# Kernel optimization log

Measured on AMD Instinct MI355X. Metric: run time of the kernel, lower is better.

The kernel has to match this reference:

```python
import jax, jax.numpy as jnp
import numpy as np

DIM = 1024
N_HEADS = 16
HEAD_DIM = DIM // N_HEADS
HIDDEN = 2816
SEQ = 4096
BATCH = 1
NORM_EPS = 1e-5


def setup_inputs() -> dict:
    key = jax.random.key(0)
    ks = jax.random.split(key, 9)
    s = 1.0 / np.sqrt(DIM)
    return {
        "x": jax.random.normal(ks[0], (BATCH, SEQ, DIM), jnp.float32),
        "wq": jax.random.normal(ks[1], (DIM, DIM), jnp.float32) * s,
        "wk": jax.random.normal(ks[2], (DIM, DIM), jnp.float32) * s,
        "wv": jax.random.normal(ks[3], (DIM, DIM), jnp.float32) * s,
        "wo": jax.random.normal(ks[4], (DIM, DIM), jnp.float32) * s,
        "w1": jax.random.normal(ks[5], (DIM, HIDDEN), jnp.float32) * s,
        "w2": jax.random.normal(ks[6], (HIDDEN, DIM), jnp.float32) / np.sqrt(HIDDEN),
        "w3": jax.random.normal(ks[7], (DIM, HIDDEN), jnp.float32) * s,
        "g_attn_norm": jnp.ones((DIM,), jnp.float32),
        "g_ffn_norm": jnp.ones((DIM,), jnp.float32),
    }


def rmsnorm(x, g):
    # x: [b, s, d]; compute in fp32 as in the torch module, then cast back
    xf = x.astype(jnp.float32)
    n = xf * jax.lax.rsqrt(jnp.mean(xf * xf, axis=-1, keepdims=True) + NORM_EPS)
    return n.astype(x.dtype) * g


def attention(x, wq, wk, wv, wo):
    b, s, _ = x.shape
    q = (x @ wq).reshape(b, s, N_HEADS, HEAD_DIM).transpose(0, 2, 1, 3)  # [b,h,s,hd]
    k = (x @ wk).reshape(b, s, N_HEADS, HEAD_DIM).transpose(0, 2, 1, 3)
    v = (x @ wv).reshape(b, s, N_HEADS, HEAD_DIM).transpose(0, 2, 1, 3)
    scores = jnp.einsum("bhqd,bhkd->bhqk", q, k) / np.sqrt(HEAD_DIM)
    causal = jnp.tril(jnp.ones((s, s), bool))
    scores = jnp.where(causal, scores, -jnp.inf)
    probs = jax.nn.softmax(scores.astype(jnp.float32), axis=-1).astype(q.dtype)
    out = jnp.einsum("bhqk,bhkd->bhqd", probs, v)
    out = out.transpose(0, 2, 1, 3).reshape(b, s, DIM)
    return out @ wo


def feed_forward(x, w1, w2, w3):
    return (jax.nn.silu(x @ w1) * (x @ w3)) @ w2


def reference(x, wq, wk, wv, wo, w1, w2, w3, g_attn_norm, g_ffn_norm):
    h = x + attention(rmsnorm(x, g_attn_norm), wq, wk, wv, wo)
    out = h + feed_forward(rmsnorm(h, g_ffn_norm), w1, w2, w3)
    return out
```

## Files before the change

### kernel.cpp

```cpp
#include <hip/hip_runtime.h>
#include <stdint.h>


typedef unsigned short u16;
typedef unsigned int u32;
typedef __attribute__((ext_vector_type(8))) short short8;
typedef __attribute__((ext_vector_type(4))) float f32x4;

#define GLD16(G, L) __builtin_amdgcn_global_load_lds( \
    (__attribute__((address_space(1))) void*)(G),      \
    (__attribute__((address_space(3))) void*)(L), 16, 0, 0)

__device__ __forceinline__ u16 f2bf(float f) {
  u32 u = __builtin_bit_cast(u32, f);
  u32 r = u + 0x7fffu + ((u >> 16) & 1u);
  return (u16)(r >> 16);
}
__device__ __forceinline__ float bf2f(u16 b) {
  u32 u = (u32)b << 16;
  return __builtin_bit_cast(float, u);
}

__global__ __launch_bounds__(256) void k_tc4(const float* __restrict__ s0,
                                             const float* __restrict__ s1,
                                             const float* __restrict__ s2,
                                             const float* __restrict__ s3,
                                             u16* __restrict__ out, int R, int C) {
  const int z = blockIdx.z;
  const float* in = (z == 0) ? s0 : (z == 1) ? s1 : (z == 2) ? s2 : s3;
  u16* o = out + (size_t)z * R * C;
  __shared__ float t[32][33];
  const int tx = threadIdx.x & 31, ty = threadIdx.x >> 5;
  const int c0 = blockIdx.x * 32, r0 = blockIdx.y * 32;
#pragma unroll
  for (int i = 0; i < 32; i += 8)
    t[ty + i][tx] = in[(size_t)(r0 + ty + i) * C + (c0 + tx)];
  __syncthreads();
#pragma unroll
  for (int i = 0; i < 32; i += 8)
    o[(size_t)(c0 + ty + i) * R + (r0 + tx)] = f2bf(t[tx][ty + i]);
}

__global__ __launch_bounds__(256) void k_rms(const float* __restrict__ x,
                                             const float* __restrict__ g,
                                             u16* __restrict__ o) {
  const int row = blockIdx.x, tid = threadIdx.x;
  const float4 v = ((const float4*)(x + (size_t)row * 1024))[tid];
  float ss = v.x * v.x + v.y * v.y + v.z * v.z + v.w * v.w;
#pragma unroll
  for (int ofs = 32; ofs > 0; ofs >>= 1) ss += __shfl_xor(ss, ofs);
  __shared__ float red[4];
  if ((tid & 63) == 0) red[tid >> 6] = ss;
  __syncthreads();
  const float s = rsqrtf((red[0] + red[1] + red[2] + red[3]) * (1.f / 1024.f) + 1e-5f);
  const float4 gv = ((const float4*)g)[tid];
  u32 lo = (u32)f2bf(v.x * s * gv.x) | ((u32)f2bf(v.y * s * gv.y) << 16);
  u32 hi = (u32)f2bf(v.z * s * gv.z) | ((u32)f2bf(v.w * s * gv.w) << 16);
  *(uint2*)(o + (size_t)row * 1024 + tid * 4) = make_uint2(lo, hi);
}

template <int EPI, int TN>
__global__ __launch_bounds__(256) void k_gemm(const u16* __restrict__ A,
                                              const u16* __restrict__ Bt,
                                              u16* __restrict__ Obf,
                                              float* __restrict__ Of,
                                              const float* __restrict__ Rz,
                                              int M, int N, int K) {
  constexpr int NFR = TN / 32;
  __shared__ __align__(16) u16 As[128 * 32];
  __shared__ __align__(16) u16 Bs[TN * 32];
  const int tid = threadIdx.x;
  const int lane = tid & 63, wave = tid >> 6;
  const int wr = wave >> 1, wc = wave & 1;
  const int li = lane & 15, lg = lane >> 4;
  const int row0 = blockIdx.y * 128, col0 = blockIdx.x * TN;

  f32x4 acc[4][NFR] = {};
  const int sr = tid >> 2, sc = (tid & 3) * 8;
  const u16* ag = A + (size_t)(row0 + sr) * K + sc;
  const u16* bg = Bt + (size_t)(col0 + sr) * K + sc;
  u16* al = As + tid * 8;
  u16* bl = Bs + tid * 8;
  const size_t rstep = (size_t)64 * K;

  for (int k0 = 0; k0 < K; k0 += 32) {
    __syncthreads();
    GLD16(ag + k0, al);
    GLD16(ag + rstep + k0, al + 2048);
    GLD16(bg + k0, bl);
    if constexpr (TN == 128) GLD16(bg + rstep + k0, bl + 2048);
    __syncthreads();
    short8 af[4], bfr[NFR];
#pragma unroll
    for (int m = 0; m < 4; ++m)
      af[m] = *(const short8*)(As + (wr * 64 + m * 16 + li) * 32 + lg * 8);
#pragma unroll
    for (int n = 0; n < NFR; ++n)
      bfr[n] = *(const short8*)(Bs + (wc * (TN / 2) + n * 16 + li) * 32 + lg * 8);
#pragma unroll
    for (int m = 0; m < 4; ++m)
#pragma unroll
      for (int n = 0; n < NFR; ++n)
        acc[m][n] = __builtin_amdgcn_mfma_f32_16x16x32_bf16(af[m], bfr[n], acc[m][n], 0, 0, 0);
  }

#pragma unroll
  for (int m = 0; m < 4; ++m) {
    const int row = row0 + wr * 64 + m * 16 + lg * 4;
#pragma unroll
    for (int n = 0; n < NFR; ++n) {
      const int col = col0 + wc * (TN / 2) + n * 16 + li;
#pragma unroll
      for (int r = 0; r < 4; ++r) {
        const size_t idx = (size_t)(row + r) * N + col;
        if (EPI == 0) Obf[idx] = f2bf(acc[m][n][r]);
        else          Of[idx] = acc[m][n][r] + Rz[idx];
      }
    }
  }
}

__global__ __launch_bounds__(256) void k_ffn13(const u16* __restrict__ A,
                                               const u16* __restrict__ B1,
                                               const u16* __restrict__ B3,
                                               u16* __restrict__ O,
                                               int M, int N, int K) {
  __shared__ __align__(16) u16 As[128 * 32];
  __shared__ __align__(16) u16 B1s[64 * 32];
  __shared__ __align__(16) u16 B3s[64 * 32];
  const int tid = threadIdx.x;
  const int lane = tid & 63, wave = tid >> 6;
  const int wr = wave >> 1, wc = wave & 1;
  const int li = lane & 15, lg = lane >> 4;
  const int row0 = blockIdx.y * 128, col0 = blockIdx.x * 64;

  f32x4 a1[4][2] = {}, a3[4][2] = {};
  const int sr = tid >> 2, sc = (tid & 3) * 8;
  const u16* ag = A + (size_t)(row0 + sr) * K + sc;
  const u16* b1g = B1 + (size_t)(col0 + sr) * K + sc;
  const u16* b3g = B3 + (size_t)(col0 + sr) * K + sc;
  u16* al = As + tid * 8;
  u16* b1l = B1s + tid * 8;
  u16* b3l = B3s + tid * 8;
  const size_t rstep = (size_t)64 * K;

  for (int k0 = 0; k0 < K; k0 += 32) {
    __syncthreads();
    GLD16(ag + k0, al);
    GLD16(ag + rstep + k0, al + 2048);
    GLD16(b1g + k0, b1l);
    GLD16(b3g + k0, b3l);
    __syncthreads();
    short8 af[4], b1f[2], b3f[2];
#pragma unroll
    for (int m = 0; m < 4; ++m)
      af[m] = *(const short8*)(As + (wr * 64 + m * 16 + li) * 32 + lg * 8);
#pragma unroll
    for (int n = 0; n < 2; ++n) {
      b1f[n] = *(const short8*)(B1s + (wc * 32 + n * 16 + li) * 32 + lg * 8);
      b3f[n] = *(const short8*)(B3s + (wc * 32 + n * 16 + li) * 32 + lg * 8);
    }
#pragma unroll
    for (int m = 0; m < 4; ++m)
#pragma unroll
      for (int n = 0; n < 2; ++n) {
        a1[m][n] = __builtin_amdgcn_mfma_f32_16x16x32_bf16(af[m], b1f[n], a1[m][n], 0, 0, 0);
        a3[m][n] = __builtin_amdgcn_mfma_f32_16x16x32_bf16(af[m], b3f[n], a3[m][n], 0, 0, 0);
      }
  }

#pragma unroll
  for (int m = 0; m < 4; ++m) {
    const int row = row0 + wr * 64 + m * 16 + lg * 4;
#pragma unroll
    for (int n = 0; n < 2; ++n) {
      const int col = col0 + wc * 32 + n * 16 + li;
#pragma unroll
      for (int r = 0; r < 4; ++r) {
        const float g1 = a1[m][n][r], g3 = a3[m][n][r];
        const float sl = g1 / (1.f + __expf(-g1));
        O[(size_t)(row + r) * N + col] = f2bf(sl * g3);
      }
    }
  }
}

__global__ __launch_bounds__(256) void k_attn(const u16* __restrict__ qkv,
                                              u16* __restrict__ o) {
  const int LD = 3072;
  const int h = blockIdx.x & 15;
  const int qb = 63 - (blockIdx.x >> 4);
  const int q0 = qb * 64;
  const int tid = threadIdx.x, lane = tid & 63, w = tid >> 6;
  const int li = lane & 15, lg = lane >> 4;
  const int swzB = (li & 7) << 4;

  __shared__ __align__(16) u16 Ks[64 * 64];
  __shared__ __align__(16) u16 Vt[64 * 64];
  __shared__ __align__(16) u16 Ps[4 * 16 * 64];

  const int qrow = q0 + w * 16 + li;
  const u16* qp = qkv + (size_t)qrow * LD + h * 64;
  short8 qf0, qf1;
#pragma unroll
  for (int j = 0; j < 8; ++j) {
    qf0[j] = (short)(__builtin_bit_cast(u32, bf2f(qp[lg * 8 + j]) * 0.125f) >> 16);
    qf1[j] = (short)(__builtin_bit_cast(u32, bf2f(qp[32 + lg * 8 + j]) * 0.125f) >> 16);
  }

  const int krow = w * 16 + (lane >> 3);
  const int kcol = ((lane & 7) ^ (lane >> 3)) * 8;
  const u16* kg = qkv + 1024 + h * 64 + kcol;
  u16* klds0 = Ks + (w * 2 + 0) * 512 + lane * 8;
  u16* klds1 = Ks + (w * 2 + 1) * 512 + lane * 8;

  const int vd0 = (tid & 31) * 2;
  const int vkq = tid >> 5;
  const u16* vg = qkv + 2048 + h * 64 + vd0;
  u32* vl0 = (u32*)(Vt + (size_t)vd0 * 64 + (((vkq * 16) ^ ((vd0 & 7) << 4)) >> 1));
  u32* vl1 = (u32*)(Vt + (size_t)(vd0 + 1) * 64 + (((vkq * 16) ^ (((vd0 + 1) & 7) << 4)) >> 1));

  u16* pw = Ps + w * 1024 + li * 64;

  float msm = -1e30f, lsm = 0.f;
  f32x4 accO[4] = {};
  u32 vld[8];

  {
    const u16* vp = vg;
#pragma unroll
    for (int i = 0; i < 8; ++i) vld[i] = *(const u32*)(vp + (size_t)(vkq * 8 + i) * LD);
  }

  for (int k0 = 0; k0 <= q0; k0 += 64) {
    __syncthreads();
    GLD16(kg + (size_t)(k0 + krow) * LD, klds0);
    GLD16(kg + (size_t)(k0 + krow + 8) * LD, klds1);
    {
      u32 lo0 = (vld[0] & 0xffffu) | (vld[1] << 16);
      u32 lo1 = (vld[2] & 0xffffu) | (vld[3] << 16);
      u32 lo2 = (vld[4] & 0xffffu) | (vld[5] << 16);
      u32 lo3 = (vld[6] & 0xffffu) | (vld[7] << 16);
      u32 hi0 = (vld[0] >> 16) | (vld[1] & 0xffff0000u);
      u32 hi1 = (vld[2] >> 16) | (vld[3] & 0xffff0000u);
      u32 hi2 = (vld[4] >> 16) | (vld[5] & 0xffff0000u);
      u32 hi3 = (vld[6] >> 16) | (vld[7] & 0xffff0000u);
      *(uint4*)vl0 = make_uint4(lo0, lo1, lo2, lo3);
      *(uint4*)vl1 = make_uint4(hi0, hi1, hi2, hi3);
    }
    __syncthreads();
    if (k0 + 64 <= q0) {
      const u16* vp = vg + (size_t)(k0 + 64) * LD;
#pragma unroll
      for (int i = 0; i < 8; ++i) vld[i] = *(const u32*)(vp + (size_t)(vkq * 8 + i) * LD);
    }

    f32x4 st[4];
#pragma unroll
    for (int f = 0; f < 4; ++f) {
      const u16* kp = Ks + (size_t)(f * 16 + li) * 64;
      const short8 ka0 = *(const short8*)(kp + (((lg * 16) ^ swzB) >> 1));
      const short8 ka1 = *(const short8*)(kp + (((64 + lg * 16) ^ swzB) >> 1));
      f32x4 z = {};
      z = __builtin_amdgcn_mfma_f32_16x16x32_bf16(ka0, qf0, z, 0, 0, 0);
      st[f] = __builtin_amdgcn_mfma_f32_16x16x32_bf16(ka1, qf1, z, 0, 0, 0);
    }

    float sv[16];
    float mloc = -1e30f;
    if (k0 < q0) {
#pragma unroll
      for (int f = 0; f < 4; ++f)
#pragma unroll
        for (int r = 0; r < 4; ++r) {
          sv[f * 4 + r] = st[f][r];
          mloc = fmaxf(mloc, sv[f * 4 + r]);
        }
    } else {
#pragma unroll
      for (int f = 0; f < 4; ++f)
#pragma unroll
        for (int r = 0; r < 4; ++r) {
          const int kg2 = k0 + f * 16 + lg * 4 + r;
          sv[f * 4 + r] = (kg2 > qrow) ? -1e30f : st[f][r];
          mloc = fmaxf(mloc, sv[f * 4 + r]);
        }
    }
    mloc = fmaxf(mloc, __shfl_xor(mloc, 16));
    mloc = fmaxf(mloc, __shfl_xor(mloc, 32));
    const float mnew = fmaxf(msm, mloc);
    const float alpha = __expf(msm - mnew);
    float psum = 0.f;
#pragma unroll
    for (int f = 0; f < 4; ++f) {
      const float p0 = __expf(sv[f * 4 + 0] - mnew);
      const float p1 = __expf(sv[f * 4 + 1] - mnew);
      const float p2 = __expf(sv[f * 4 + 2] - mnew);
      const float p3 = __expf(sv[f * 4 + 3] - mnew);
      psum += (p0 + p1) + (p2 + p3);
      const u32 lo = (u32)f2bf(p0) | ((u32)f2bf(p1) << 16);
      const u32 hi = (u32)f2bf(p2) | ((u32)f2bf(p3) << 16);
      *(uint2*)(pw + (((f * 32 + lg * 8) ^ swzB) >> 1)) = make_uint2(lo, hi);
    }
    psum += __shfl_xor(psum, 16);
    psum += __shfl_xor(psum, 32);
    lsm = lsm * alpha + psum;
    msm = mnew;
#pragma unroll
    for (int n = 0; n < 4; ++n) {
      accO[n][0] *= alpha; accO[n][1] *= alpha;
      accO[n][2] *= alpha; accO[n][3] *= alpha;
    }

#pragma unroll
    for (int kk = 0; kk < 2; ++kk) {
      const int cofs = ((kk * 64 + lg * 16) ^ swzB) >> 1;
      const short8 pf = *(const short8*)(pw + cofs);
#pragma unroll
      for (int n = 0; n < 4; ++n) {
        const short8 vf = *(const short8*)(Vt + (size_t)(n * 16 + li) * 64 + cofs);
        accO[n] = __builtin_amdgcn_mfma_f32_16x16x32_bf16(vf, pf, accO[n], 0, 0, 0);
      }
    }
  }

  const float linv = 1.f / lsm;
  u16* op = o + (size_t)(q0 + w * 16 + li) * 1024 + h * 64;
#pragma unroll
  for (int n = 0; n < 4; ++n) {
    const u32 lo = (u32)f2bf(accO[n][0] * linv) | ((u32)f2bf(accO[n][1] * linv) << 16);
    const u32 hi = (u32)f2bf(accO[n][2] * linv) | ((u32)f2bf(accO[n][3] * linv) << 16);
    *(uint2*)(op + n * 16 + lg * 4) = make_uint2(lo, hi);
  }
}

extern "C" void kernel_launch(void* const* d_in, const int* in_sizes, int n_in,
                              void* d_out, int out_size, void* d_ws, size_t ws_size,
                              hipStream_t stream) {
  const float* x  = (const float*)d_in[0];
  const float* wq = (const float*)d_in[1];
  const float* wk = (const float*)d_in[2];
  const float* wv = (const float*)d_in[3];
  const float* wo = (const float*)d_in[4];
  const float* w1 = (const float*)d_in[5];
  const float* w2 = (const float*)d_in[6];
  const float* w3 = (const float*)d_in[7];
  const float* ga = (const float*)d_in[8];
  const float* gf = (const float*)d_in[9];
  float* out = (float*)d_out;

  char* p = (char*)d_ws;
  auto take = [&](size_t n) { char* r = p; p += (n + 255) & ~(size_t)255; return r; };
  u16* wqkvo_t = (u16*)take(4096ull * 1024 * 1024 / 512 * 2);
  u16* w13_t   = (u16*)take(2ull * 2816 * 1024 * 2);
  u16* w2_t    = (u16*)take(1024ull * 2816 * 2);
  u16* xn      = (u16*)take(4096ull * 1024 * 2);
  u16* qkvb    = (u16*)take(4096ull * 3072 * 2);
  u16* atn     = (u16*)take(4096ull * 1024 * 2);
  float* hb    = (float*)take(4096ull * 1024 * 4);
  u16* hn      = (u16*)take(4096ull * 1024 * 2);
  u16* ffb     = (u16*)take(4096ull * 2816 * 2);

  u16* wqkv_t = wqkvo_t;
  u16* wo_t   = wqkvo_t + 3ull * 1024 * 1024;
  u16* w1_t   = w13_t;
  u16* w3_t   = w13_t + 2816ull * 1024;

  k_tc4<<<dim3(32, 32, 4), 256, 0, stream>>>(wq, wk, wv, wo, wqkvo_t, 1024, 1024);
  k_tc4<<<dim3(88, 32, 2), 256, 0, stream>>>(w1, w3, w1, w3, w13_t, 1024, 2816);
  k_tc4<<<dim3(32, 88, 1), 256, 0, stream>>>(w2, w2, w2, w2, w2_t, 2816, 1024);

  k_rms<<<4096, 256, 0, stream>>>(x, ga, xn);
  k_gemm<0, 128><<<dim3(24, 32), 256, 0, stream>>>(xn, wqkv_t, qkvb, nullptr, nullptr, 4096, 3072, 1024);
  k_attn<<<1024, 256, 0, stream>>>(qkvb, atn);
  k_gemm<1, 64><<<dim3(16, 32), 256, 0, stream>>>(atn, wo_t, nullptr, hb, x, 4096, 1024, 1024);
  k_rms<<<4096, 256, 0, stream>>>(hb, gf, hn);
  k_ffn13<<<dim3(44, 32), 256, 0, stream>>>(hn, w1_t, w3_t, ffb, 4096, 2816, 1024);
  k_gemm<1, 64><<<dim3(16, 32), 256, 0, stream>>>(ffb, w2_t, nullptr, out, hb, 4096, 1024, 2816);
}
```

Before: 322.9 us.

## Enlarge attention query tile to 128 rows with 8 waves and lazy rescaling

The attention kernel now processes 128 query rows per block with 512 threads, so each K/V tile loaded into LDS serves twice as many queries. The softmax switches to exp2 with log2e folded into the Q scale, and it skips the running-max rescale unless the max grows by more than 8. Conversions now use the hardware packed bf16 convert. Per-wave causal skipping avoids wasted tiles, but the larger blocks halve the grid size and may reduce occupancy.

```diff
diff --git a/kernel.cpp b/kernel.cpp
--- a/kernel.cpp
+++ b/kernel.cpp
@@ -19,6 +19,11 @@
 __device__ __forceinline__ float bf2f(u16 b) {
   u32 u = (u32)b << 16;
   return __builtin_bit_cast(float, u);
+}
+__device__ __forceinline__ u32 pk_bf16(float lo, float hi) {
+  u32 r;
+  asm("v_cvt_pk_bf16_f32 %0, %1, %2" : "=v"(r) : "v"(lo), "v"(hi));
+  return r;
 }
 
 __global__ __launch_bounds__(256) void k_tc4(const float* __restrict__ s0,
@@ -185,152 +190,151 @@
   }
 }
 
-__global__ __launch_bounds__(256) void k_attn(const u16* __restrict__ qkv,
+__global__ __launch_bounds__(512) void k_attn(const u16* __restrict__ qkv,
                                               u16* __restrict__ o) {
   const int LD = 3072;
   const int h = blockIdx.x & 15;
-  const int qb = 63 - (blockIdx.x >> 4);
-  const int q0 = qb * 64;
+  const int qb = 31 - (blockIdx.x >> 4);
+  const int q0 = qb * 128;
   const int tid = threadIdx.x, lane = tid & 63, w = tid >> 6;
   const int li = lane & 15, lg = lane >> 4;
   const int swzB = (li & 7) << 4;
 
   __shared__ __align__(16) u16 Ks[64 * 64];
   __shared__ __align__(16) u16 Vt[64 * 64];
-  __shared__ __align__(16) u16 Ps[4 * 16 * 64];
+  __shared__ __align__(16) u16 Ps[8 * 16 * 64];
 
   const int qrow = q0 + w * 16 + li;
   const u16* qp = qkv + (size_t)qrow * LD + h * 64;
+  const float QS = 0.125f * 1.44269504f;
   short8 qf0, qf1;
 #pragma unroll
   for (int j = 0; j < 8; ++j) {
-    qf0[j] = (short)(__builtin_bit_cast(u32, bf2f(qp[lg * 8 + j]) * 0.125f) >> 16);
-    qf1[j] = (short)(__builtin_bit_cast(u32, bf2f(qp[32 + lg * 8 + j]) * 0.125f) >> 16);
-  }
-
-  const int krow = w * 16 + (lane >> 3);
-  const int kcol = ((lane & 7) ^ (lane >> 3)) * 8;
-  const u16* kg = qkv + 1024 + h * 64 + kcol;
-  u16* klds0 = Ks + (w * 2 + 0) * 512 + lane * 8;
-  u16* klds1 = Ks + (w * 2 + 1) * 512 + lane * 8;
+    qf0[j] = (short)f2bf(bf2f(qp[lg * 8 + j]) * QS);
+    qf1[j] = (short)f2bf(bf2f(qp[32 + lg * 8 + j]) * QS);
+  }
+
+  const int krow = tid >> 3;
+  const u16* kg = qkv + 1024 + h * 64 + ((tid & 7) ^ (krow & 7)) * 8;
+  u16* klds = Ks + tid * 8;
 
   const int vd0 = (tid & 31) * 2;
   const int vkq = tid >> 5;
   const u16* vg = qkv + 2048 + h * 64 + vd0;
-  u32* vl0 = (u32*)(Vt + (size_t)vd0 * 64 + (((vkq * 16) ^ ((vd0 & 7) << 4)) >> 1));
-  u32* vl1 = (u32*)(Vt + (size_t)(vd0 + 1) * 64 + (((vkq * 16) ^ (((vd0 + 1) & 7) << 4)) >> 1));
+  u16* vl0 = Vt + (size_t)vd0 * 64 + (((vkq * 8) ^ ((vd0 & 7) << 4)) >> 1);
+  u16* vl1 = Vt + (size_t)(vd0 + 1) * 64 + (((vkq * 8) ^ (((vd0 + 1) & 7) << 4)) >> 1);
 
   u16* pw = Ps + w * 1024 + li * 64;
 
   float msm = -1e30f, lsm = 0.f;
   f32x4 accO[4] = {};
-  u32 vld[8];
+  u32 vld[4];
 
   {
-    const u16* vp = vg;
-#pragma unroll
-    for (int i = 0; i < 8; ++i) vld[i] = *(const u32*)(vp + (size_t)(vkq * 8 + i) * LD);
-  }
-
-  for (int k0 = 0; k0 <= q0; k0 += 64) {
-    __syncthreads();
-    GLD16(kg + (size_t)(k0 + krow) * LD, klds0);
-    GLD16(kg + (size_t)(k0 + krow + 8) * LD, klds1);
+#pragma unroll
+    for (int i = 0; i < 4; ++i) vld[i] = *(const u32*)(vg + (size_t)(vkq * 4 + i) * LD);
+  }
+
+  const int kend = q0 + 64;
+  const int wqmax = q0 + w * 16 + 15;
+  for (int k0 = 0; k0 <= kend; k0 += 64) {
+    __syncthreads();
+    GLD16(kg + (size_t)(k0 + krow) * LD, klds);
     {
       u32 lo0 = (vld[0] & 0xffffu) | (vld[1] << 16);
       u32 lo1 = (vld[2] & 0xffffu) | (vld[3] << 16);
-      u32 lo2 = (vld[4] & 0xffffu) | (vld[5] << 16);
-      u32 lo3 = (vld[6] & 0xffffu) | (vld[7] << 16);
       u32 hi0 = (vld[0] >> 16) | (vld[1] & 0xffff0000u);
       u32 hi1 = (vld[2] >> 16) | (vld[3] & 0xffff0000u);
-      u32 hi2 = (vld[4] >> 16) | (vld[5] & 0xffff0000u);
-      u32 hi3 = (vld[6] >> 16) | (vld[7] & 0xffff0000u);
-      *(uint4*)vl0 = make_uint4(lo0, lo1, lo2, lo3);
-      *(uint4*)vl1 = make_uint4(hi0, hi1, hi2, hi3);
-    }
-    __syncthreads();
-    if (k0 + 64 <= q0) {
+      *(uint2*)vl0 = make_uint2(lo0, lo1);
+      *(uint2*)vl1 = make_uint2(hi0, hi1);
+    }
+    __syncthreads();
+    if (k0 + 64 <= kend) {
       const u16* vp = vg + (size_t)(k0 + 64) * LD;
 #pragma unroll
-      for (int i = 0; i < 8; ++i) vld[i] = *(const u32*)(vp + (size_t)(vkq * 8 + i) * LD);
-    }
-
-    f32x4 st[4];
-#pragma unroll
-    for (int f = 0; f < 4; ++f) {
-      const u16* kp = Ks + (size_t)(f * 16 + li) * 64;
-      const short8 ka0 = *(const short8*)(kp + (((lg * 16) ^ swzB) >> 1));
-      const short8 ka1 = *(const short8*)(kp + (((64 + lg * 16) ^ swzB) >> 1));
-      f32x4 z = {};
-      z = __builtin_amdgcn_mfma_f32_16x16x32_bf16(ka0, qf0, z, 0, 0, 0);
-      st[f] = __builtin_amdgcn_mfma_f32_16x16x32_bf16(ka1, qf1, z, 0, 0, 0);
-    }
-
-    float sv[16];
-    float mloc = -1e30f;
-    if (k0 < q0) {
-#pragma unroll
-      for (int f = 0; f < 4; ++f)
-#pragma unroll
-        for (int r = 0; r < 4; ++r) {
-          sv[f * 4 + r] = st[f][r];
-          mloc = fmaxf(mloc, sv[f * 4 + r]);
+      for (int i = 0; i < 4; ++i) vld[i] = *(const u32*)(vp + (size_t)(vkq * 4 + i) * LD);
+    }
+
+    if (k0 <= wqmax) {
+      f32x4 st[4];
+#pragma unroll
+      for (int f = 0; f < 4; ++f) {
+        const u16* kp = Ks + (size_t)(f * 16 + li) * 64;
+        const short8 ka0 = *(const short8*)(kp + (((lg * 16) ^ swzB) >> 1));
+        const short8 ka1 = *(const short8*)(kp + (((64 + lg * 16) ^ swzB) >> 1));
+        f32x4 z = {};
+        z = __builtin_amdgcn_mfma_f32_16x16x32_bf16(ka0, qf0, z, 0, 0, 0);
+        st[f] = __builtin_amdgcn_mfma_f32_16x16x32_bf16(ka1, qf1, z, 0, 0, 0);
+      }
+
+      float sv[16];
+      float mloc = -1e30f;
+      if (k0 + 63 <= q0 + w * 16) {
+#pragma unroll
+        for (int f = 0; f < 4; ++f)
+#pragma unroll
+          for (int r = 0; r < 4; ++r) {
+            sv[f * 4 + r] = st[f][r];
+            mloc = fmaxf(mloc, sv[f * 4 + r]);
+          }
+      } else {
+#pragma unroll
+        for (int f = 0; f < 4; ++f)
+#pragma unroll
+          for (int r = 0; r < 4; ++r) {
+            const int kg2 = k0 + f * 16 + lg * 4 + r;
+            sv[f * 4 + r] = (kg2 > qrow) ? -1e30f : st[f][r];
+            mloc = fmaxf(mloc, sv[f * 4 + r]);
+          }
+      }
+      mloc = fmaxf(mloc, __shfl_xor(mloc, 16));
+      mloc = fmaxf(mloc, __shfl_xor(mloc, 32));
+      if (!__all(mloc - msm <= 8.0f)) {
+        const float mnew = fmaxf(msm, mloc);
+        const float alpha = __builtin_amdgcn_exp2f(msm - mnew);
+        lsm *= alpha;
+#pragma unroll
+        for (int n = 0; n < 4; ++n) {
+          accO[n][0] *= alpha; accO[n][1] *= alpha;
+          accO[n][2] *= alpha; accO[n][3] *= alpha;
         }
-    } else {
-#pragma unroll
-      for (int f = 0; f < 4; ++f)
-#pragma unroll
-        for (int r = 0; r < 4; ++r) {
-          const int kg2 = k0 + f * 16 + lg * 4 + r;
-          sv[f * 4 + r] = (kg2 > qrow) ? -1e30f : st[f][r];
-          mloc = fmaxf(mloc, sv[f * 4 + r]);
+        msm = mnew;
+      }
+      float psum = 0.f;
+#pragma unroll
+      for (int f = 0; f < 4; ++f) {
+        const float p0 = __builtin_amdgcn_exp2f(sv[f * 4 + 0] - msm);
+        const float p1 = __builtin_amdgcn_exp2f(sv[f * 4 + 1] - msm);
+        const float p2 = __builtin_amdgcn_exp2f(sv[f * 4 + 2] - msm);
+        const float p3 = __builtin_amdgcn_exp2f(sv[f * 4 + 3] - msm);
+        psum += (p0 + p1) + (p2 + p3);
+        *(uint2*)(pw + (((f * 32 + lg * 8) ^ swzB) >> 1)) =
+            make_uint2(pk_bf16(p0, p1), pk_bf16(p2, p3));
+      }
+      psum += __shfl_xor(psum, 16);
+      psum += __shfl_xor(psum, 32);
+      lsm += psum;
+
+#pragma unroll
+      for (int kk = 0; kk < 2; ++kk) {
+        const int cofs = ((kk * 64 + lg * 16) ^ swzB) >> 1;
+        const short8 pf = *(const short8*)(pw + cofs);
+#pragma unroll
+        for (int n = 0; n < 4; ++n) {
+          const short8 vf = *(const short8*)(Vt + (size_t)(n * 16 + li) * 64 + cofs);
+          accO[n] = __builtin_amdgcn_mfma_f32_16x16x32_bf16(vf, pf, accO[n], 0, 0, 0);
         }
-    }
-    mloc = fmaxf(mloc, __shfl_xor(mloc, 16));
-    mloc = fmaxf(mloc, __shfl_xor(mloc, 32));
-    const float mnew = fmaxf(msm, mloc);
-    const float alpha = __expf(msm - mnew);
-    float psum = 0.f;
-#pragma unroll
-    for (int f = 0; f < 4; ++f) {
-      const float p0 = __expf(sv[f * 4 + 0] - mnew);
-      const float p1 = __expf(sv[f * 4 + 1] - mnew);
-      const float p2 = __expf(sv[f * 4 + 2] - mnew);
-      const float p3 = __expf(sv[f * 4 + 3] - mnew);
-      psum += (p0 + p1) + (p2 + p3);
-      const u32 lo = (u32)f2bf(p0) | ((u32)f2bf(p1) << 16);
-      const u32 hi = (u32)f2bf(p2) | ((u32)f2bf(p3) << 16);
-      *(uint2*)(pw + (((f * 32 + lg * 8) ^ swzB) >> 1)) = make_uint2(lo, hi);
-    }
-    psum += __shfl_xor(psum, 16);
-    psum += __shfl_xor(psum, 32);
-    lsm = lsm * alpha + psum;
-    msm = mnew;
-#pragma unroll
-    for (int n = 0; n < 4; ++n) {
-      accO[n][0] *= alpha; accO[n][1] *= alpha;
-      accO[n][2] *= alpha; accO[n][3] *= alpha;
-    }
-
-#pragma unroll
-    for (int kk = 0; kk < 2; ++kk) {
-      const int cofs = ((kk * 64 + lg * 16) ^ swzB) >> 1;
-      const short8 pf = *(const short8*)(pw + cofs);
-#pragma unroll
-      for (int n = 0; n < 4; ++n) {
-        const short8 vf = *(const short8*)(Vt + (size_t)(n * 16 + li) * 64 + cofs);
-        accO[n] = __builtin_amdgcn_mfma_f32_16x16x32_bf16(vf, pf, accO[n], 0, 0, 0);
       }
     }
   }
 
   const float linv = 1.f / lsm;
-  u16* op = o + (size_t)(q0 + w * 16 + li) * 1024 + h * 64;
+  u16* op = o + (size_t)qrow * 1024 + h * 64;
 #pragma unroll
   for (int n = 0; n < 4; ++n) {
-    const u32 lo = (u32)f2bf(accO[n][0] * linv) | ((u32)f2bf(accO[n][1] * linv) << 16);
-    const u32 hi = (u32)f2bf(accO[n][2] * linv) | ((u32)f2bf(accO[n][3] * linv) << 16);
-    *(uint2*)(op + n * 16 + lg * 4) = make_uint2(lo, hi);
+    *(uint2*)(op + n * 16 + lg * 4) =
+        make_uint2(pk_bf16(accO[n][0] * linv, accO[n][1] * linv),
+                   pk_bf16(accO[n][2] * linv, accO[n][3] * linv));
   }
 }
 
@@ -351,7 +355,7 @@
 
   char* p = (char*)d_ws;
   auto take = [&](size_t n) { char* r = p; p += (n + 255) & ~(size_t)255; return r; };
-  u16* wqkvo_t = (u16*)take(4096ull * 1024 * 1024 / 512 * 2);
+  u16* wqkvo_t = (u16*)take(4ull * 1024 * 1024 * 2);
   u16* w13_t   = (u16*)take(2ull * 2816 * 1024 * 2);
   u16* w2_t    = (u16*)take(1024ull * 2816 * 2);
   u16* xn      = (u16*)take(4096ull * 1024 * 2);
@@ -372,7 +376,7 @@
 
   k_rms<<<4096, 256, 0, stream>>>(x, ga, xn);
   k_gemm<0, 128><<<dim3(24, 32), 256, 0, stream>>>(xn, wqkv_t, qkvb, nullptr, nullptr, 4096, 3072, 1024);
-  k_attn<<<1024, 256, 0, stream>>>(qkvb, atn);
+  k_attn<<<512, 512, 0, stream>>>(qkvb, atn);
   k_gemm<1, 64><<<dim3(16, 32), 256, 0, stream>>>(atn, wo_t, nullptr, hb, x, 4096, 1024, 1024);
   k_rms<<<4096, 256, 0, stream>>>(hb, gf, hn);
   k_ffn13<<<dim3(44, 32), 256, 0, stream>>>(hn, w1_t, w3_t, ffb, 4096, 2816, 1024);
```

Result: faster. 311.4 us (-3.6%).
